# Kernel optimization log

Measured on AMD Instinct MI355X. Metric: run time of the kernel, lower is better.

## Reference

```python
import jax, jax.numpy as jnp
import numpy as np

B, A, T = 256, 512, 21
DIM = 128
SC = 6
NHEAD, HD = 4, DIM // 4

def conv1d_relu(x, w, b, stride=2):
    # x: (N, C, L), w: (O, I, K)
    y = jax.lax.conv_general_dilated(x, w, (stride,), 'SAME', dimension_numbers=('NCH', 'OIH', 'NCH'))
    return jax.nn.relu(y + b[None, :, None])

def to_vector(feat, vm):
    vec_mask = vm[..., :-1] & vm[..., 1:]
    while vec_mask.ndim < feat.ndim:
        vec_mask = vec_mask[..., None]
    return jnp.where(vec_mask, feat[:, :, 1:] - feat[:, :, :-1], jnp.zeros_like(feat[:, :, 1:]))

def setup_inputs():
    key = jax.random.key(0)
    ks = jax.random.split(key, 24)
    f32 = jnp.float32
    inp = {}
    inp['position'] = jax.random.normal(ks[0], (B, A, T, 2), f32)
    inp['heading'] = jax.random.normal(ks[1], (B, A, T), f32)
    inp['velocity'] = jax.random.normal(ks[2], (B, A, T, 2), f32)
    inp['shape'] = jax.random.uniform(ks[3], (B, A, T, 2), f32)
    inp['current_state'] = jax.random.normal(ks[4], (B, SC), f32)
    inp['category'] = jax.random.randint(ks[5], (B, A), 0, 4)
    inp['valid_mask'] = jax.random.randint(ks[6], (B, A, T), 0, 2).astype(bool)
    # history encoder (CNN) params: 9 -> 32 -> 64 -> 128 channels, k=3, stride 2
    inp['conv1_w'] = jax.random.normal(ks[7], (32, 9, 3), f32) * 0.1
    inp['conv1_b'] = jnp.zeros((32,), f32)
    inp['conv2_w'] = jax.random.normal(ks[8], (64, 32, 3), f32) * 0.1
    inp['conv2_b'] = jnp.zeros((64,), f32)
    inp['conv3_w'] = jax.random.normal(ks[9], (128, 64, 3), f32) * 0.1
    inp['conv3_b'] = jnp.zeros((128,), f32)
    # StateAttentionEncoder params
    inp['se_w'] = jax.random.normal(ks[10], (SC, DIM), f32) * 0.02   # per-channel Linear(1,dim) weights
    inp['se_b'] = jnp.zeros((SC, DIM), f32)
    inp['pos_embed'] = jax.random.normal(ks[11], (1, SC, DIM), f32) * 0.02
    inp['query'] = jax.random.normal(ks[12], (1, 1, DIM), f32) * 0.02
    inp['in_proj_w'] = jax.random.normal(ks[13], (3 * DIM, DIM), f32) * (1.0 / np.sqrt(DIM))
    inp['in_proj_b'] = jnp.zeros((3 * DIM,), f32)
    inp['out_proj_w'] = jax.random.normal(ks[14], (DIM, DIM), f32) * (1.0 / np.sqrt(DIM))
    inp['out_proj_b'] = jnp.zeros((DIM,), f32)
    inp['type_emb'] = jax.random.normal(ks[15], (4, DIM), f32) * 0.02
    return inp

def reference(position, heading, velocity, shape, current_state, category, valid_mask,
              conv1_w, conv1_b, conv2_w, conv2_b, conv3_w, conv3_b,
              se_w, se_b, pos_embed, query, in_proj_w, in_proj_b, out_proj_w, out_proj_b,
              type_emb):
    # --- build per-step agent features (B, A, T-1, 9) ---
    heading_vec = to_vector(heading, valid_mask)
    valid_mask_vec = valid_mask[..., 1:] & valid_mask[..., :-1]
    agent_feature = jnp.concatenate([
        to_vector(position, valid_mask),
        to_vector(velocity, valid_mask),
        jnp.stack([jnp.cos(heading_vec), jnp.sin(heading_vec)], axis=-1),
        shape[:, :, 1:],
        valid_mask_vec.astype(jnp.float32)[..., None],
    ], axis=-1)
    bs, nA, Tm1, C = agent_feature.shape
    x = agent_feature.reshape(bs * nA, Tm1, C).transpose(0, 2, 1)  # (N, 9, T-1)
    # --- history CNN encoder (applied to all rows, then masked; same math as boolean gather/scatter) ---
    h = conv1d_relu(x, conv1_w, conv1_b)
    h = conv1d_relu(h, conv2_w, conv2_b)
    h = conv1d_relu(h, conv3_w, conv3_b)
    enc = h.mean(axis=-1)  # (N, DIM)
    valid_agent = valid_mask.any(-1).reshape(-1)
    x_agent = jnp.where(valid_agent[:, None], enc, 0.0).reshape(bs, nA, DIM)
    # --- ego state attention encoder (eval mode: no token dropout) ---
    ego = current_state[:, :SC]
    x_embed = ego[:, :, None] * se_w[None] + se_b[None] + pos_embed  # (B, SC, DIM)
    Wq, Wk, Wv = in_proj_w[:DIM], in_proj_w[DIM:2 * DIM], in_proj_w[2 * DIM:]
    bq, bk, bv = in_proj_b[:DIM], in_proj_b[DIM:2 * DIM], in_proj_b[2 * DIM:]
    q = (query[0, 0] @ Wq.T + bq).reshape(NHEAD, HD)             # (H, D)
    k = (x_embed @ Wk.T + bk).reshape(bs, SC, NHEAD, HD)          # (B, S, H, D)
    v = (x_embed @ Wv.T + bv).reshape(bs, SC, NHEAD, HD)
    scores = jnp.einsum('hd,bshd->bhs', q, k) * (1.0 / np.sqrt(HD))
    attn = jax.nn.softmax(scores, axis=-1)
    o = jnp.einsum('bhs,bshd->bhd', attn, v).reshape(bs, DIM)
    x_ego = o @ out_proj_w.T + out_proj_b                         # (B, DIM)
    x_agent = x_agent.at[:, 0].set(x_ego)
    # --- type embedding add ---
    return x_agent + type_emb[category]
```

## Files before the change

kernel.cpp:

```cpp
#include <hip/hip_runtime.h>
#include <hip/hip_bf16.h>


#define BB 256
#define AAG 512
#define TT 21
#define NAG (BB * AAG)

typedef __hip_bfloat16 bf16;
typedef __attribute__((ext_vector_type(8))) short s8v;
typedef __attribute__((ext_vector_type(4))) float f4v;

__device__ int g_dtype;
__device__ int g_mask_mode;
__device__ __align__(16) short g_w1p[32 * 64];
__device__ __align__(16) short g_w2p[64 * 96];
__device__ __align__(16) short g_w3p[128 * 192];
__device__ __align__(16) float g_b1[32];
__device__ __align__(16) float g_b2[64];
__device__ __align__(16) float g_b3[128];

template <int DT>
__device__ __forceinline__ float ldf(const void* p, long i) {
    if (DT) return __bfloat162float(((const bf16*)p)[i]);
    return ((const float*)p)[i];
}
template <int DT>
__device__ __forceinline__ void stf(void* p, long i, float v) {
    if (DT) ((bf16*)p)[i] = __float2bfloat16(v);
    else    ((float*)p)[i] = v;
}
__device__ __forceinline__ unsigned short f2bu(float x) {
    bf16 b = __float2bfloat16(x);
    union { bf16 b; unsigned short u; } cv; cv.b = b; return cv.u;
}
__device__ __forceinline__ float bu2f(unsigned short u) {
    union { unsigned int i; float f; } cv; cv.i = ((unsigned int)u) << 16; return cv.f;
}
__device__ __forceinline__ bool mask_at(const void* p, long i, int mode) {
    if (mode == 0) return ((const int*)p)[i] != 0;
    if (mode == 1) return ((const unsigned char*)p)[i] != 0;
    if (mode == 2) return ((const float*)p)[i] != 0.f;
    return (((const unsigned short*)p)[i] & 0x7fff) != 0;
}

__global__ void detect_kernel(const unsigned int* __restrict__ pw,
                              const unsigned char* __restrict__ m) {
    __shared__ int cls[4];
    __shared__ int mv;
    __shared__ int good;
    int tid = threadIdx.x;
    if (tid < 4) cls[tid] = 0;
    if (tid == 0) { mv = 0; good = 0; }
    __syncthreads();
    int g = 0;
    for (int i = tid; i < 1024; i += 256) {
        unsigned int w = pw[i];
        unsigned int h0 = w & 0xffffu, h1 = w >> 16;
        unsigned int e0 = (h0 >> 7) & 0xff, e1 = (h1 >> 7) & 0xff;
        if (h0 == 0 || (e0 >= 90 && e0 <= 160)) g++;
        if (h1 == 0 || (e1 >= 90 && e1 <= 160)) g++;
    }
    atomicAdd(&good, g);
    int l0 = 0, l1 = 0, l2 = 0, l3 = 0, lm = 0;
    for (int i = tid; i < 4096; i += 256) {
        int v = m[i];
        if (v) {
            switch (i & 3) { case 0: l0 = 1; break; case 1: l1 = 1; break;
                             case 2: l2 = 1; break; default: l3 = 1; }
            if (v > lm) lm = v;
        }
    }
    if (l0) atomicOr(&cls[0], 1);
    if (l1) atomicOr(&cls[1], 1);
    if (l2) atomicOr(&cls[2], 1);
    if (l3) atomicOr(&cls[3], 1);
    atomicMax(&mv, lm);
    __syncthreads();
    if (tid == 0) {
        g_dtype = (good >= 1740) ? 1 : 0;
        int mode;
        if (!cls[1] && !cls[2] && !cls[3]) mode = 0;
        else if (!cls[0] && !cls[1])       mode = 2;
        else if (mv <= 1)                  mode = 1;
        else                               mode = 3;
        g_mask_mode = mode;
    }
}

template <int DT>
__global__ void prep_weights_kernel(const void* __restrict__ w1, const void* __restrict__ b1,
                                    const void* __restrict__ w2, const void* __restrict__ b2,
                                    const void* __restrict__ w3, const void* __restrict__ b3) {
    if (g_dtype != DT) return;
    int tid = blockIdx.x * blockDim.x + threadIdx.x;
    int nt = gridDim.x * blockDim.x;
    for (int i = tid; i < 32 * 64; i += nt) {
        int oc = i >> 6, k = i & 63, tap = k >> 4, ic = k & 15;
        float v = (tap < 3 && ic < 9) ? ldf<DT>(w1, oc * 27 + ic * 3 + tap) : 0.f;
        g_w1p[i] = (short)f2bu(v);
    }
    for (int i = tid; i < 64 * 96; i += nt) {
        int oc = i / 96, k = i % 96, tap = k >> 5, ic = k & 31;
        g_w2p[i] = (short)f2bu(ldf<DT>(w2, oc * 96 + ic * 3 + tap));
    }
    for (int i = tid; i < 128 * 192; i += nt) {
        int oc = i / 192, k = i % 192, tap = k >> 6, ic = k & 63;
        g_w3p[i] = (short)f2bu(ldf<DT>(w3, oc * 192 + ic * 3 + tap));
    }
    for (int i = tid; i < 32; i += nt) g_b1[i] = ldf<DT>(b1, i);
    for (int i = tid; i < 64; i += nt) g_b2[i] = ldf<DT>(b2, i);
    for (int i = tid; i < 128; i += nt) g_b3[i] = ldf<DT>(b3, i);
}

#define FEAT_RS 24
#define FEAT_AS 528
#define H1_RS 40
#define H1_AS 440
#define H2_RS 72
#define H2_AS 504
#define C3_AS 384
#define OFF_H1 8448
#define OFF_H2 15488
#define OFF_VALID 47104
#define SMEM_BYTES 47168

#define MFMA16(a, b, c) __builtin_amdgcn_mfma_f32_16x16x32_bf16((a), (b), (c), 0, 0, 0)

template <int DT>
__global__ __launch_bounds__(256) void stage1_kernel(
    const void* __restrict__ pos, const void* __restrict__ heading,
    const void* __restrict__ vel, const void* __restrict__ shp,
    const void* __restrict__ vmask, const int* __restrict__ category,
    const void* __restrict__ type_emb, void* __restrict__ out) {
    if (g_dtype != DT) return;
    __shared__ __align__(16) char smem[SMEM_BYTES];
    short* feat = (short*)smem;
    short* h1 = (short*)smem + OFF_H1;
    short* h2 = (short*)smem + OFF_H2;
    short* c3 = (short*)smem;
    int* s_valid = (int*)(smem + OFF_VALID);

    const int tid = threadIdx.x;
    const int wave = tid >> 6, lane = tid & 63;
    const int col = lane & 15, quad = lane >> 4;
    const long agent0 = (long)blockIdx.x * 16;
    const int mode = g_mask_mode;

    if (tid < 16) s_valid[tid] = 0;
    {
        unsigned int* h1u = (unsigned int*)h1;
        int ag = tid >> 4, c = tid & 15;
        h1u[ag * 220 + 200 + c] = 0;
        unsigned int* h2u = (unsigned int*)h2;
        for (int i = tid; i < 1024; i += 256) {
            int a2 = i >> 6, r = (i >> 5) & 1, cc = i & 31;
            h2u[a2 * 252 + r * 216 + cc] = 0;
        }
    }
    __syncthreads();

    for (int idx = tid; idx < 16 * 22; idx += 256) {
        int ag = idx / 22, t = idx % 22;
        short* row = feat + ag * FEAT_AS + t * FEAT_RS;
        if (t >= 20) {
            *(uint4*)row = make_uint4(0, 0, 0, 0);
            *(uint4*)(row + 8) = make_uint4(0, 0, 0, 0);
            if (t == 20) {
                long base = (agent0 + ag) * TT + 20;
                if (mask_at(vmask, base, mode)) atomicOr(&s_valid[ag], 1);
            }
        } else {
            long base = (agent0 + ag) * TT + t;
            bool vmt = mask_at(vmask, base, mode);
            if (vmt) atomicOr(&s_valid[ag], 1);
            bool m2 = vmt && mask_at(vmask, base + 1, mode);
            float px0 = ldf<DT>(pos, base * 2),     py0 = ldf<DT>(pos, base * 2 + 1);
            float px1 = ldf<DT>(pos, base * 2 + 2), py1 = ldf<DT>(pos, base * 2 + 3);
            float vx0 = ldf<DT>(vel, base * 2),     vy0 = ldf<DT>(vel, base * 2 + 1);
            float vx1 = ldf<DT>(vel, base * 2 + 2), vy1 = ldf<DT>(vel, base * 2 + 3);
            float hh0 = ldf<DT>(heading, base), hh1 = ldf<DT>(heading, base + 1);
            float sx = ldf<DT>(shp, base * 2 + 2), sy = ldf<DT>(shp, base * 2 + 3);
            float dh = m2 ? (hh1 - hh0) : 0.f;
            float sn = sinf(dh), cn = cosf(dh);
            unsigned int p0 = f2bu(m2 ? px1 - px0 : 0.f) | ((unsigned int)f2bu(m2 ? py1 - py0 : 0.f) << 16);
            unsigned int p1 = f2bu(m2 ? vx1 - vx0 : 0.f) | ((unsigned int)f2bu(m2 ? vy1 - vy0 : 0.f) << 16);
            unsigned int p2 = f2bu(cn) | ((unsigned int)f2bu(sn) << 16);
            unsigned int p3 = f2bu(sx) | ((unsigned int)f2bu(sy) << 16);
            unsigned int p4 = (unsigned int)f2bu(m2 ? 1.f : 0.f);
            *(uint4*)row = make_uint4(p0, p1, p2, p3);
            *(uint4*)(row + 8) = make_uint4(p4, 0, 0, 0);
        }
    }
    __syncthreads();

    {
        int Mt = wave >> 1;
        int oc = Mt * 16 + col;
        s8v a0 = *(const s8v*)(g_w1p + oc * 64 + quad * 8);
        s8v a1 = *(const s8v*)(g_w1p + oc * 64 + 32 + quad * 8);
        int k0 = quad * 8, k1 = 32 + quad * 8;
        int tap0 = k0 >> 4, ic0 = k0 & 15;
        int tap1 = k1 >> 4, ic1 = k1 & 15;
        int ocr = Mt * 16 + quad * 4;
        f4v bia = *(const f4v*)(g_b1 + ocr);
#pragma unroll
        for (int i = 0; i < 5; i++) {
            int Nt = (wave & 1) * 5 + i;
            int n = Nt * 16 + col;
            int ag = n / 10, p = n % 10;
            const short* bb = feat + ag * FEAT_AS + 2 * p * FEAT_RS;
            s8v b0 = *(const s8v*)(bb + tap0 * FEAT_RS + ic0);
            s8v b1 = *(const s8v*)(bb + tap1 * FEAT_RS + ic1);
            f4v acc = {0.f, 0.f, 0.f, 0.f};
            acc = MFMA16(a0, b0, acc);
            acc = MFMA16(a1, b1, acc);
            unsigned int lo = f2bu(fmaxf(acc[0] + bia[0], 0.f)) | ((unsigned int)f2bu(fmaxf(acc[1] + bia[1], 0.f)) << 16);
            unsigned int hi = f2bu(fmaxf(acc[2] + bia[2], 0.f)) | ((unsigned int)f2bu(fmaxf(acc[3] + bia[3], 0.f)) << 16);
            *(uint2*)(h1 + ag * H1_AS + p * H1_RS + ocr) = make_uint2(lo, hi);
        }
    }
    __syncthreads();

    {
        int Mt = wave;
        int oc = Mt * 16 + col;
        s8v a[3];
#pragma unroll
        for (int ks = 0; ks < 3; ks++)
            a[ks] = *(const s8v*)(g_w2p + oc * 96 + ks * 32 + quad * 8);
        int ocr = Mt * 16 + quad * 4;
        f4v bia = *(const f4v*)(g_b2 + ocr);
#pragma unroll
        for (int Nt = 0; Nt < 5; Nt++) {
            int n = Nt * 16 + col;
            int ag = n / 5, p = n % 5;
            f4v acc = {0.f, 0.f, 0.f, 0.f};
#pragma unroll
            for (int ks = 0; ks < 3; ks++) {
                s8v b = *(const s8v*)(h1 + ag * H1_AS + (2 * p + ks) * H1_RS + quad * 8);
                acc = MFMA16(a[ks], b, acc);
            }
            unsigned int lo = f2bu(fmaxf(acc[0] + bia[0], 0.f)) | ((unsigned int)f2bu(fmaxf(acc[1] + bia[1], 0.f)) << 16);
            unsigned int hi = f2bu(fmaxf(acc[2] + bia[2], 0.f)) | ((unsigned int)f2bu(fmaxf(acc[3] + bia[3], 0.f)) << 16);
            *(uint2*)(h2 + ag * H2_AS + (p + 1) * H2_RS + ocr) = make_uint2(lo, hi);
        }
    }
    __syncthreads();

#pragma unroll
    for (int m2 = 0; m2 < 2; m2++) {
        int Mt = wave * 2 + m2;
        int oc = Mt * 16 + col;
        s8v a[6];
#pragma unroll
        for (int ks = 0; ks < 6; ks++)
            a[ks] = *(const s8v*)(g_w3p + oc * 192 + ks * 32 + quad * 8);
        int ocr = Mt * 16 + quad * 4;
        f4v bia = *(const f4v*)(g_b3 + ocr);
#pragma unroll
        for (int Nt = 0; Nt < 3; Nt++) {
            int n = Nt * 16 + col;
            int ag = n / 3, p = n % 3;
            f4v acc = {0.f, 0.f, 0.f, 0.f};
#pragma unroll
            for (int ks = 0; ks < 6; ks++) {
                int kg = ks * 32 + quad * 8;
                int tap = kg >> 6, ic = kg & 63;
                s8v b = *(const s8v*)(h2 + ag * H2_AS + (2 * p + tap) * H2_RS + ic);
                acc = MFMA16(a[ks], b, acc);
            }
            unsigned int lo = f2bu(fmaxf(acc[0] + bia[0], 0.f)) | ((unsigned int)f2bu(fmaxf(acc[1] + bia[1], 0.f)) << 16);
            unsigned int hi = f2bu(fmaxf(acc[2] + bia[2], 0.f)) | ((unsigned int)f2bu(fmaxf(acc[3] + bia[3], 0.f)) << 16);
            *(uint2*)(c3 + ag * C3_AS + p * 128 + ocr) = make_uint2(lo, hi);
        }
    }
    __syncthreads();

    {
        int ag = tid >> 4;
        int ocg = (tid & 15) * 8;
        s8v x0 = *(const s8v*)(c3 + ag * C3_AS + ocg);
        s8v x1 = *(const s8v*)(c3 + ag * C3_AS + 128 + ocg);
        s8v x2 = *(const s8v*)(c3 + ag * C3_AS + 256 + ocg);
        int valid = s_valid[ag];
        long agl = agent0 + ag;
        int cat = category[agl];
#pragma unroll
        for (int j = 0; j < 8; j++) {
            float m = (bu2f((unsigned short)x0[j]) + bu2f((unsigned short)x1[j]) +
                       bu2f((unsigned short)x2[j])) * (1.f / 3.f);
            if (!valid) m = 0.f;
            float te = ldf<DT>(type_emb, cat * 128 + ocg + j);
            stf<DT>(out, agl * 128 + ocg + j, m + te);
        }
    }
}

template <int DT>
__global__ __launch_bounds__(128) void stage2_kernel(
    const void* __restrict__ cs, const int* __restrict__ category,
    const void* __restrict__ se_w, const void* __restrict__ se_b,
    const void* __restrict__ pe, const void* __restrict__ query,
    const void* __restrict__ ipw, const void* __restrict__ ipb,
    const void* __restrict__ opw, const void* __restrict__ opb,
    const void* __restrict__ type_emb, void* __restrict__ out) {
    if (g_dtype != DT) return;
    int b = blockIdx.x, d = threadIdx.x;
    __shared__ float s_xe[6][128];
    __shared__ float s_qu[128];
    __shared__ float s_q[128];
    __shared__ float s_k[6][128];
    __shared__ float s_v[6][128];
    __shared__ float s_att[4][6];
    __shared__ float s_o[128];

    s_qu[d] = ldf<DT>(query, d);
#pragma unroll
    for (int s = 0; s < 6; s++) {
        float ego = ldf<DT>(cs, b * 6 + s);
        s_xe[s][d] = fmaf(ego, ldf<DT>(se_w, s * 128 + d),
                          ldf<DT>(se_b, s * 128 + d) + ldf<DT>(pe, s * 128 + d));
    }
    __syncthreads();

    float accq = ldf<DT>(ipb, d);
    float bk = ldf<DT>(ipb, 128 + d), bv = ldf<DT>(ipb, 256 + d);
    float acck[6], accv[6];
#pragma unroll
    for (int s = 0; s < 6; s++) { acck[s] = bk; accv[s] = bv; }
    for (int e = 0; e < 128; e++) {
        float wqe = ldf<DT>(ipw, (long)d * 128 + e);
        accq = fmaf(s_qu[e], wqe, accq);
        float wke = ldf<DT>(ipw, (long)(128 + d) * 128 + e);
        float wve = ldf<DT>(ipw, (long)(256 + d) * 128 + e);
#pragma unroll
        for (int s = 0; s < 6; s++) {
            float xe = s_xe[s][e];
            acck[s] = fmaf(xe, wke, acck[s]);
            accv[s] = fmaf(xe, wve, accv[s]);
        }
    }
    s_q[d] = accq;
#pragma unroll
    for (int s = 0; s < 6; s++) { s_k[s][d] = acck[s]; s_v[s][d] = accv[s]; }
    __syncthreads();

    if (d < 4) {
        float sc[6];
        float mx = -1e30f;
#pragma unroll
        for (int s = 0; s < 6; s++) {
            float t = 0.f;
            for (int q = 0; q < 32; q++) t = fmaf(s_q[d * 32 + q], s_k[s][d * 32 + q], t);
            t *= 0.17677669529663687f;
            sc[s] = t;
            mx = fmaxf(mx, t);
        }
        float sum = 0.f;
#pragma unroll
        for (int s = 0; s < 6; s++) { sc[s] = expf(sc[s] - mx); sum += sc[s]; }
        float inv = 1.f / sum;
#pragma unroll
        for (int s = 0; s < 6; s++) s_att[d][s] = sc[s] * inv;
    }
    __syncthreads();

    {
        int h = d >> 5;
        float o = 0.f;
#pragma unroll
        for (int s = 0; s < 6; s++) o = fmaf(s_att[h][s], s_v[s][d], o);
        s_o[d] = o;
    }
    __syncthreads();

    float acc = ldf<DT>(opb, d);
    for (int e = 0; e < 128; e++) acc = fmaf(s_o[e], ldf<DT>(opw, (long)d * 128 + e), acc);
    int cat = category[(long)b * AAG];
    stf<DT>(out, (long)b * AAG * 128 + d, acc + ldf<DT>(type_emb, cat * 128 + d));
}

extern "C" void kernel_launch(void* const* d_in, const int* in_sizes, int n_in,
                              void* d_out, int out_size, void* d_ws, size_t ws_size,
                              hipStream_t stream) {
    const void* position      = d_in[0];
    const void* heading       = d_in[1];
    const void* velocity      = d_in[2];
    const void* shape         = d_in[3];
    const void* current_state = d_in[4];
    const int*  category      = (const int*)d_in[5];
    const void* valid_mask    = d_in[6];
    const void* conv1_w = d_in[7];
    const void* conv1_b = d_in[8];
    const void* conv2_w = d_in[9];
    const void* conv2_b = d_in[10];
    const void* conv3_w = d_in[11];
    const void* conv3_b = d_in[12];
    const void* se_w    = d_in[13];
    const void* se_b    = d_in[14];
    const void* pos_embed = d_in[15];
    const void* query     = d_in[16];
    const void* in_proj_w = d_in[17];
    const void* in_proj_b = d_in[18];
    const void* out_proj_w = d_in[19];
    const void* out_proj_b = d_in[20];
    const void* type_emb   = d_in[21];

    hipLaunchKernelGGL(detect_kernel, dim3(1), dim3(256), 0, stream,
                       (const unsigned int*)position, (const unsigned char*)valid_mask);

    hipLaunchKernelGGL(prep_weights_kernel<0>, dim3(64), dim3(256), 0, stream,
                       conv1_w, conv1_b, conv2_w, conv2_b, conv3_w, conv3_b);
    hipLaunchKernelGGL(prep_weights_kernel<1>, dim3(64), dim3(256), 0, stream,
                       conv1_w, conv1_b, conv2_w, conv2_b, conv3_w, conv3_b);

    hipLaunchKernelGGL(stage1_kernel<0>, dim3(NAG / 16), dim3(256), 0, stream,
                       position, heading, velocity, shape, valid_mask, category, type_emb, d_out);
    hipLaunchKernelGGL(stage1_kernel<1>, dim3(NAG / 16), dim3(256), 0, stream,
                       position, heading, velocity, shape, valid_mask, category, type_emb, d_out);

    hipLaunchKernelGGL(stage2_kernel<0>, dim3(BB), dim3(128), 0, stream,
                       current_state, category, se_w, se_b, pos_embed, query,
                       in_proj_w, in_proj_b, out_proj_w, out_proj_b, type_emb, d_out);
    hipLaunchKernelGGL(stage2_kernel<1>, dim3(BB), dim3(128), 0, stream,
                       current_state, category, se_w, se_b, pos_embed, query,
                       in_proj_w, in_proj_b, out_proj_w, out_proj_b, type_emb, d_out);
}
```

Measured before the change: 321.6 us.

## Shrink LDS footprint, vectorize global loads/stores, simplify MFMA N-mapping

```diff
diff --git a/kernel.cpp b/kernel.cpp
--- a/kernel.cpp
+++ b/kernel.cpp
@@ -36,6 +36,15 @@
 }
 __device__ __forceinline__ float bu2f(unsigned short u) {
     union { unsigned int i; float f; } cv; cv.i = ((unsigned int)u) << 16; return cv.f;
+}
+template <int DT>
+__device__ __forceinline__ float2 ldf2(const void* p, long i) {
+    if (DT) {
+        unsigned int u = *(const unsigned int*)((const bf16*)p + i);
+        return make_float2(bu2f((unsigned short)(u & 0xffffu)),
+                           bu2f((unsigned short)(u >> 16)));
+    }
+    return *(const float2*)((const float*)p + i);
 }
 __device__ __forceinline__ bool mask_at(const void* p, long i, int mode) {
     if (mode == 0) return ((const int*)p)[i] != 0;
@@ -114,16 +123,15 @@
 }
 
 #define FEAT_RS 24
-#define FEAT_AS 528
+#define FEAT_AS 568
 #define H1_RS 40
 #define H1_AS 440
 #define H2_RS 72
 #define H2_AS 504
-#define C3_AS 384
-#define OFF_H1 8448
-#define OFF_H2 15488
-#define OFF_VALID 47104
-#define SMEM_BYTES 47168
+#define C3_AS 392
+#define OFF_H1 9088
+#define OFF_VALID 32256
+#define SMEM_BYTES 32320
 
 #define MFMA16(a, b, c) __builtin_amdgcn_mfma_f32_16x16x32_bf16((a), (b), (c), 0, 0, 0)
 
@@ -136,9 +144,9 @@
     if (g_dtype != DT) return;
     __shared__ __align__(16) char smem[SMEM_BYTES];
     short* feat = (short*)smem;
-    short* h1 = (short*)smem + OFF_H1;
-    short* h2 = (short*)smem + OFF_H2;
-    short* c3 = (short*)smem;
+    short* h1   = (short*)smem + OFF_H1;
+    short* h2   = (short*)smem;
+    short* c3   = (short*)smem + OFF_H1;
     int* s_valid = (int*)(smem + OFF_VALID);
 
     const int tid = threadIdx.x;
@@ -150,13 +158,7 @@
     if (tid < 16) s_valid[tid] = 0;
     {
         unsigned int* h1u = (unsigned int*)h1;
-        int ag = tid >> 4, c = tid & 15;
-        h1u[ag * 220 + 200 + c] = 0;
-        unsigned int* h2u = (unsigned int*)h2;
-        for (int i = tid; i < 1024; i += 256) {
-            int a2 = i >> 6, r = (i >> 5) & 1, cc = i & 31;
-            h2u[a2 * 252 + r * 216 + cc] = 0;
-        }
+        h1u[(tid >> 4) * 220 + 200 + (tid & 15)] = 0;
     }
     __syncthreads();
 
@@ -175,18 +177,17 @@
             bool vmt = mask_at(vmask, base, mode);
             if (vmt) atomicOr(&s_valid[ag], 1);
             bool m2 = vmt && mask_at(vmask, base + 1, mode);
-            float px0 = ldf<DT>(pos, base * 2),     py0 = ldf<DT>(pos, base * 2 + 1);
-            float px1 = ldf<DT>(pos, base * 2 + 2), py1 = ldf<DT>(pos, base * 2 + 3);
-            float vx0 = ldf<DT>(vel, base * 2),     vy0 = ldf<DT>(vel, base * 2 + 1);
-            float vx1 = ldf<DT>(vel, base * 2 + 2), vy1 = ldf<DT>(vel, base * 2 + 3);
+            float2 pa = ldf2<DT>(pos, base * 2), pb = ldf2<DT>(pos, base * 2 + 2);
+            float2 va = ldf2<DT>(vel, base * 2), vb = ldf2<DT>(vel, base * 2 + 2);
             float hh0 = ldf<DT>(heading, base), hh1 = ldf<DT>(heading, base + 1);
-            float sx = ldf<DT>(shp, base * 2 + 2), sy = ldf<DT>(shp, base * 2 + 3);
+            float2 sv = ldf2<DT>(shp, base * 2 + 2);
             float dh = m2 ? (hh1 - hh0) : 0.f;
-            float sn = sinf(dh), cn = cosf(dh);
-            unsigned int p0 = f2bu(m2 ? px1 - px0 : 0.f) | ((unsigned int)f2bu(m2 ? py1 - py0 : 0.f) << 16);
-            unsigned int p1 = f2bu(m2 ? vx1 - vx0 : 0.f) | ((unsigned int)f2bu(m2 ? vy1 - vy0 : 0.f) << 16);
+            float sn, cn;
+            __sincosf(dh, &sn, &cn);
+            unsigned int p0 = f2bu(m2 ? pb.x - pa.x : 0.f) | ((unsigned int)f2bu(m2 ? pb.y - pa.y : 0.f) << 16);
+            unsigned int p1 = f2bu(m2 ? vb.x - va.x : 0.f) | ((unsigned int)f2bu(m2 ? vb.y - va.y : 0.f) << 16);
             unsigned int p2 = f2bu(cn) | ((unsigned int)f2bu(sn) << 16);
-            unsigned int p3 = f2bu(sx) | ((unsigned int)f2bu(sy) << 16);
+            unsigned int p3 = f2bu(sv.x) | ((unsigned int)f2bu(sv.y) << 16);
             unsigned int p4 = (unsigned int)f2bu(m2 ? 1.f : 0.f);
             *(uint4*)row = make_uint4(p0, p1, p2, p3);
             *(uint4*)(row + 8) = make_uint4(p4, 0, 0, 0);
@@ -204,12 +205,12 @@
         int tap1 = k1 >> 4, ic1 = k1 & 15;
         int ocr = Mt * 16 + quad * 4;
         f4v bia = *(const f4v*)(g_b1 + ocr);
+        int ag = col;
+        const short* agbase = feat + ag * FEAT_AS;
 #pragma unroll
         for (int i = 0; i < 5; i++) {
-            int Nt = (wave & 1) * 5 + i;
-            int n = Nt * 16 + col;
-            int ag = n / 10, p = n % 10;
-            const short* bb = feat + ag * FEAT_AS + 2 * p * FEAT_RS;
+            int p = (wave & 1) * 5 + i;
+            const short* bb = agbase + 2 * p * FEAT_RS;
             s8v b0 = *(const s8v*)(bb + tap0 * FEAT_RS + ic0);
             s8v b1 = *(const s8v*)(bb + tap1 * FEAT_RS + ic1);
             f4v acc = {0.f, 0.f, 0.f, 0.f};
@@ -223,6 +224,11 @@
     __syncthreads();
 
     {
+        unsigned int* h2u = (unsigned int*)h2;
+        for (int i = tid; i < 1024; i += 256) {
+            int a2 = i >> 6, r = (i >> 5) & 1, cc = i & 31;
+            h2u[a2 * 252 + r * 216 + cc] = 0;
+        }
         int Mt = wave;
         int oc = Mt * 16 + col;
         s8v a[3];
@@ -231,10 +237,9 @@
             a[ks] = *(const s8v*)(g_w2p + oc * 96 + ks * 32 + quad * 8);
         int ocr = Mt * 16 + quad * 4;
         f4v bia = *(const f4v*)(g_b2 + ocr);
-#pragma unroll
-        for (int Nt = 0; Nt < 5; Nt++) {
-            int n = Nt * 16 + col;
-            int ag = n / 5, p = n % 5;
+        int ag = col;
+#pragma unroll
+        for (int p = 0; p < 5; p++) {
             f4v acc = {0.f, 0.f, 0.f, 0.f};
 #pragma unroll
             for (int ks = 0; ks < 3; ks++) {
@@ -258,10 +263,9 @@
             a[ks] = *(const s8v*)(g_w3p + oc * 192 + ks * 32 + quad * 8);
         int ocr = Mt * 16 + quad * 4;
         f4v bia = *(const f4v*)(g_b3 + ocr);
-#pragma unroll
-        for (int Nt = 0; Nt < 3; Nt++) {
-            int n = Nt * 16 + col;
-            int ag = n / 3, p = n % 3;
+        int ag = col;
+#pragma unroll
+        for (int p = 0; p < 3; p++) {
             f4v acc = {0.f, 0.f, 0.f, 0.f};
 #pragma unroll
             for (int ks = 0; ks < 6; ks++) {
@@ -280,19 +284,34 @@
     {
         int ag = tid >> 4;
         int ocg = (tid & 15) * 8;
-        s8v x0 = *(const s8v*)(c3 + ag * C3_AS + ocg);
-        s8v x1 = *(const s8v*)(c3 + ag * C3_AS + 128 + ocg);
-        s8v x2 = *(const s8v*)(c3 + ag * C3_AS + 256 + ocg);
+        const short* cb = c3 + ag * C3_AS;
+        s8v x0 = *(const s8v*)(cb + ocg);
+        s8v x1 = *(const s8v*)(cb + 128 + ocg);
+        s8v x2 = *(const s8v*)(cb + 256 + ocg);
         int valid = s_valid[ag];
         long agl = agent0 + ag;
         int cat = category[agl];
+        float vals[8];
 #pragma unroll
         for (int j = 0; j < 8; j++) {
             float m = (bu2f((unsigned short)x0[j]) + bu2f((unsigned short)x1[j]) +
                        bu2f((unsigned short)x2[j])) * (1.f / 3.f);
-            if (!valid) m = 0.f;
-            float te = ldf<DT>(type_emb, cat * 128 + ocg + j);
-            stf<DT>(out, agl * 128 + ocg + j, m + te);
+            vals[j] = valid ? m : 0.f;
+        }
+        if (DT) {
+            s8v te = *(const s8v*)((const bf16*)type_emb + (long)cat * 128 + ocg);
+            s8v o;
+#pragma unroll
+            for (int j = 0; j < 8; j++)
+                o[j] = (short)f2bu(vals[j] + bu2f((unsigned short)te[j]));
+            *(s8v*)((bf16*)out + agl * 128 + ocg) = o;
+        } else {
+            const float4* tep = (const float4*)((const float*)type_emb + (long)cat * 128 + ocg);
+            float4 t0 = tep[0], t1 = tep[1];
+            float4 o0 = make_float4(vals[0] + t0.x, vals[1] + t0.y, vals[2] + t0.z, vals[3] + t0.w);
+            float4 o1 = make_float4(vals[4] + t1.x, vals[5] + t1.y, vals[6] + t1.z, vals[7] + t1.w);
+            float4* op = (float4*)((float*)out + agl * 128 + ocg);
+            op[0] = o0; op[1] = o1;
         }
     }
 }
```

Result: faster. 304.5 us (-5.3%).
